# Kernel optimization log

Measured on AMD Instinct MI355X. Metric: run time of the kernel, lower is better.

The kernel has to match this reference:

```python
import jax, jax.numpy as jnp
import numpy as np

B, CIN, COUT, RES, WDIM, K, GN_GROUPS = 8, 512, 512, 64, 512, 3, 32


def setup_inputs() -> dict:
    key = jax.random.key(0)
    ks = jax.random.split(key, 6)
    return dict(
        x=jax.random.normal(ks[0], (B, CIN, RES, RES), jnp.float32),
        w=jax.random.normal(ks[1], (B, WDIM), jnp.float32),
        noise=jax.random.normal(ks[2], (B, 1, RES, RES), jnp.float32),
        weight=jax.random.normal(ks[3], (COUT, CIN, K, K), jnp.float32),
        bias=jnp.zeros((COUT,), jnp.float32),
        affine_W=jax.random.normal(ks[4], (3 * CIN, WDIM), jnp.float32),
        affine_b=jnp.ones((3 * CIN,), jnp.float32),  # bias_init=1
        gn_weight=jnp.ones((CIN,), jnp.float32),
        gn_bias=jnp.zeros((CIN,), jnp.float32),
        gamma=jnp.full((1, COUT, 1, 1), 1e-5, jnp.float32),  # layer_scale_init
        noise_strength=jnp.asarray(0.1, jnp.float32),
    )


def _group_norm_f32(x, weight, bias, groups=GN_GROUPS, eps=1e-5):
    # GroupNorm_float32: normalize in float32, cast back to x.dtype
    b, c, h, w = x.shape
    xf = x.astype(jnp.float32).reshape(b, groups, c // groups, h, w)
    mu = xf.mean(axis=(2, 3, 4), keepdims=True)
    var = xf.var(axis=(2, 3, 4), keepdims=True)
    xn = ((xf - mu) * jax.lax.rsqrt(var + eps)).reshape(b, c, h, w)
    return (xn * weight[None, :, None, None] + bias[None, :, None, None]).astype(x.dtype)


def reference(x, w, noise, weight, bias, affine_W, affine_b, gn_weight, gn_bias, gamma, noise_strength):
    b, cin, h, wd = x.shape
    cout, _, kh, kw = weight.shape
    # StyleSplit: FullyConnectedLayer (weight scaled by 1/sqrt(in_features)) then m1*m2+m3
    s = w @ (affine_W.T / jnp.sqrt(jnp.float32(w.shape[1]))) + affine_b  # [B, 3*Cin]
    m1, m2, m3 = jnp.split(s, 3, axis=1)
    styles = m1 * m2 + m3  # [B, Cin]
    # residual path: GroupNorm (float32) first
    xn = _group_norm_f32(x, gn_weight, gn_bias)
    # modulated_conv2d (fused path): per-sample modulate + demodulate
    wmod = weight[None] * styles[:, None, :, None, None]                 # [B,Cout,Cin,K,K]
    dcoef = jax.lax.rsqrt(jnp.sum(jnp.square(wmod), axis=(2, 3, 4)) + 1e-8)  # [B,Cout]
    wmod = wmod * dcoef[:, :, None, None, None]
    # grouped conv with groups = batch (StyleGAN batch-as-groups trick)
    xg = xn.reshape(1, b * cin, h, wd)
    wg = wmod.reshape(b * cout, cin, kh, kw)
    pad = kh // 2
    y = jax.lax.conv_general_dilated(
        xg, wg, window_strides=(1, 1), padding=[(pad, pad), (pad, pad)],
        dimension_numbers=('NCHW', 'OIHW', 'NCHW'), feature_group_count=b)
    y = y.reshape(b, cout, h, wd)
    # noise injection
    y = y + noise * noise_strength
    # fused bias + lrelu with gain = bias_def_gain['lrelu'] * gain = sqrt(2) * 2
    act_gain = np.sqrt(2.0) * 2.0
    y = jax.nn.leaky_relu(y + bias[None, :, None, None], 0.2) * act_gain
    # layer-scale + residual (residual uses the normalized x) * sqrt(2)
    y = (gamma * y + xn) * np.sqrt(2.0)
    return y
```

## Files before the change

### kernel.cpp

```cpp
#include <hip/hip_runtime.h>
#include <hip/hip_bf16.h>

typedef short short8 __attribute__((ext_vector_type(8)));
typedef float f32x4 __attribute__((ext_vector_type(4)));

#define SWZ(c) (((c) & 3) ^ (((c) >> 2) & 3))

static __device__ __forceinline__ unsigned short f2bf(float f) {
    union { float f; unsigned u; } v; v.f = f;
    unsigned r = v.u + 0x7FFFu + ((v.u >> 16) & 1u);
    return (unsigned short)(r >> 16);
}

static __device__ __forceinline__ void gload16(const void* g, void* l) {
    __builtin_amdgcn_global_load_lds(
        (const __attribute__((address_space(1))) unsigned int*)g,
        (__attribute__((address_space(3))) unsigned int*)l, 16, 0, 0);
}

__global__ __launch_bounds__(256) void stylesk(
    const float* __restrict__ w, const float* __restrict__ affW,
    const float* __restrict__ affb, float* __restrict__ styles)
{
    int ch = blockIdx.x, b = blockIdx.y;
    int lane = threadIdx.x & 63, wv = threadIdx.x >> 6;
    float wr[8];
    const float* wb = w + b * 512 + lane * 8;
#pragma unroll
    for (int r = 0; r < 8; ++r) wr[r] = wb[r];
    for (int ii = 0; ii < 16; ++ii) {
        int i = ch * 64 + wv * 16 + ii;
        float d[3];
#pragma unroll
        for (int jj = 0; jj < 3; ++jj) {
            const float* a = affW + (size_t)(jj * 512 + i) * 512 + lane * 8;
            float dd = 0.f;
#pragma unroll
            for (int r = 0; r < 8; ++r) dd += wr[r] * a[r];
            for (int off = 32; off; off >>= 1) dd += __shfl_xor(dd, off);
            d[jj] = dd;
        }
        if (lane == 0) {
            const float inv = 0.044194173824159216f;
            float s0 = d[0] * inv + affb[i];
            float s1 = d[1] * inv + affb[512 + i];
            float s2 = d[2] * inv + affb[1024 + i];
            styles[b * 512 + i] = s0 * s1 + s2;
        }
    }
}

__global__ __launch_bounds__(256) void gnstats(
    const float* __restrict__ x, float* __restrict__ meanv, float* __restrict__ rstdv)
{
    int bx = blockIdx.x, t = threadIdx.x;
    const float4* p = (const float4*)(x + (size_t)bx * 65536);
    float s = 0.f, q = 0.f;
#pragma unroll 4
    for (int k = 0; k < 64; ++k) {
        float4 v = p[t + (k << 8)];
        s += v.x + v.y + v.z + v.w;
        q += v.x * v.x + v.y * v.y + v.z * v.z + v.w * v.w;
    }
    for (int off = 32; off; off >>= 1) { s += __shfl_xor(s, off); q += __shfl_xor(q, off); }
    __shared__ float rs[4], rq[4];
    if ((t & 63) == 0) { rs[t >> 6] = s; rq[t >> 6] = q; }
    __syncthreads();
    if (t == 0) {
        float S = rs[0] + rs[1] + rs[2] + rs[3];
        float Q = rq[0] + rq[1] + rq[2] + rq[3];
        float mu = S * (1.f / 65536.f);
        float var = Q * (1.f / 65536.f) - mu * mu;
        meanv[bx] = mu;
        rstdv[bx] = rsqrtf(var + 1e-5f);
    }
}

__global__ __launch_bounds__(256) void dcoefk(
    const float* __restrict__ weight, const float* __restrict__ styles,
    float* __restrict__ dcoef)
{
    __shared__ float st2[8 * 512];
    __shared__ float red[32];
    int co = blockIdx.x, t = threadIdx.x;
    for (int i = t; i < 4096; i += 256) { float s = styles[i]; st2[i] = s * s; }
    __syncthreads();
    float p[8] = {0, 0, 0, 0, 0, 0, 0, 0};
#pragma unroll
    for (int half = 0; half < 2; ++half) {
        int ci = t * 2 + half;
        const float* wp = weight + ((size_t)co * 512 + ci) * 9;
        float wsq = 0.f;
#pragma unroll
        for (int k = 0; k < 9; ++k) wsq += wp[k] * wp[k];
#pragma unroll
        for (int b = 0; b < 8; ++b) p[b] += wsq * st2[b * 512 + ci];
    }
    int lane = t & 63, wv = t >> 6;
#pragma unroll
    for (int b = 0; b < 8; ++b) {
        float v = p[b];
        for (int off = 32; off; off >>= 1) v += __shfl_xor(v, off);
        if (lane == 0) red[wv * 8 + b] = v;
    }
    __syncthreads();
    if (t < 8) {
        float s = red[t] + red[8 + t] + red[16 + t] + red[24 + t];
        dcoef[t * 512 + co] = rsqrtf(s + 1e-8f);
    }
}

__global__ __launch_bounds__(256) void packk(
    const float* __restrict__ weight, unsigned short* __restrict__ wpk)
{
    __shared__ float ld[9 * 128];
    int co = blockIdx.x, c4 = blockIdx.y, t = threadIdx.x;
    const float* src = weight + (size_t)co * 4608 + c4 * 1152;
    for (int f = t; f < 1152; f += 256)
        ld[(f % 9) * 128 + (f / 9)] = src[f];
    __syncthreads();
    unsigned short* dst = wpk + (size_t)co * 4608 + c4 * 128;
    for (int f = t; f < 1152; f += 256) {
        int tap = f >> 7, ci = f & 127;
        dst[tap * 512 + ci] = f2bf(ld[tap * 128 + ci]);
    }
}

__global__ __launch_bounds__(256) void modpack(
    const float* __restrict__ x, const float* __restrict__ styles,
    const float* __restrict__ gnw, const float* __restrict__ gnb,
    const float* __restrict__ meanv, const float* __restrict__ rstdv,
    unsigned short* __restrict__ xm)
{
    __shared__ float sA[512], sB[512];
    __shared__ unsigned short tr[32 * 520];
    int t = threadIdx.x;
    int px0 = blockIdx.x * 32, b = blockIdx.y;
    for (int i = t; i < 512; i += 256) {
        int g = i >> 4;
        float mu = meanv[b * 32 + g], r = rstdv[b * 32 + g];
        float st = styles[b * 512 + i];
        float a = r * gnw[i];
        sA[i] = a * st;
        sB[i] = (gnb[i] - mu * a) * st;
    }
    __syncthreads();
    int p = t & 31, cb = t >> 5;
    const float* xb = x + (size_t)b * 512 * 4096 + px0 + p;
#pragma unroll 4
    for (int it = 0; it < 64; ++it) {
        int ci = cb + (it << 3);
        float v = xb[(size_t)ci * 4096];
        tr[p * 520 + ci] = f2bf(v * sA[ci] + sB[ci]);
    }
    __syncthreads();
    int gran = t & 63;
#pragma unroll
    for (int k = 0; k < 8; ++k) {
        int pl = k * 4 + (t >> 6);
        short8 v = *(const short8*)&tr[pl * 520 + gran * 8];
        *(short8*)&xm[((size_t)(b * 4096 + px0 + pl) << 9) + gran * 8] = v;
    }
}

__global__ __launch_bounds__(256, 2) void conv3(
    const unsigned short* __restrict__ xm, const unsigned short* __restrict__ wpk,
    const unsigned short* __restrict__ zp,
    const float* __restrict__ x, const float* __restrict__ noise,
    const float* __restrict__ bias, const float* __restrict__ gnw,
    const float* __restrict__ gnb, const float* __restrict__ gamma,
    const float* __restrict__ dcoef, const float* __restrict__ meanv,
    const float* __restrict__ rstdv, const float* __restrict__ nsp,
    float* __restrict__ out)
{
    __shared__ unsigned short in_lds[4 * 66 * 32];
    __shared__ unsigned short w_lds[3 * 128 * 32];
    const int tid = threadIdx.x, lane = tid & 63, wv = tid >> 6;
    const int ct = blockIdx.x, pt = blockIdx.y, b = blockIdx.z;
    const int co0 = ct * 128;
    const int wm = wv >> 1, wn = wv & 1;
    const int lm = lane & 15, lg = lane >> 4;

    if (tid < 32) {
        int r = tid >> 3, cI = ((tid >> 2) & 1) * 65, g = tid & 3;
        *(short8*)((char*)in_lds + r * 4224 + cI * 64 + g * 16) = (short8)0;
    }

    const int h0 = pt * 2;
    const int imgrow = h0 - 1 + wv;
    const bool rowok = (unsigned)imgrow < 64u;
    const unsigned short* isrc[4];
    char* idst[4];
#pragma unroll
    for (int q = 0; q < 4; ++q) {
        int lin = q * 64 + lane;
        int c1 = lin >> 2, g = lin & 3;
        int gs = g ^ SWZ(c1 + 1);
        isrc[q] = xm + (((size_t)(b * 4096 + imgrow * 64 + c1)) << 9) + gs * 8;
        idst[q] = (char*)in_lds + wv * 4224 + 64 + q * 1024;
    }
    const unsigned short* wsrc[6];
    char* wdst[6];
#pragma unroll
    for (int j = 0; j < 6; ++j) {
        int gid = wv * 384 + j * 64 + lane;
        int dx = gid >> 9, co = (gid >> 2) & 127, g = gid & 3;
        wsrc[j] = wpk + (size_t)(co0 + co) * 4608 + dx * 512 + (g ^ SWZ(co)) * 8;
        wdst[j] = (char*)w_lds + (wv * 384 + j * 64) * 16;
    }

    f32x4 acc[4][4];
#pragma unroll
    for (int m = 0; m < 4; ++m)
#pragma unroll
        for (int n = 0; n < 4; ++n) acc[m][n] = (f32x4){0.f, 0.f, 0.f, 0.f};

    for (int cc = 0; cc < 16; ++cc) {
        __syncthreads();
#pragma unroll
        for (int q = 0; q < 4; ++q)
            gload16(rowok ? (const void*)(isrc[q] + cc * 32) : (const void*)zp, idst[q]);
#pragma unroll
        for (int dy = 0; dy < 3; ++dy) {
            if (dy) __syncthreads();
#pragma unroll
            for (int j = 0; j < 6; ++j)
                gload16(wsrc[j] + dy * 1536 + cc * 32, wdst[j]);
            __syncthreads();
#pragma unroll
            for (int dx = 0; dx < 3; ++dx) {
                short8 af[4], bf[4];
#pragma unroll
                for (int m = 0; m < 4; ++m) {
                    int col = wm * 64 + m * 16 + lm;
                    af[m] = *(const short8*)((char*)w_lds +
                            (dx * 128 + col) * 64 + (lg ^ SWZ(col)) * 16);
                }
#pragma unroll
                for (int n = 0; n < 4; ++n) {
                    int c = n * 16 + lm + dx;
                    bf[n] = *(const short8*)((char*)in_lds +
                            (wn + dy) * 4224 + c * 64 + (lg ^ SWZ(c)) * 16);
                }
#pragma unroll
                for (int m = 0; m < 4; ++m)
#pragma unroll
                    for (int n = 0; n < 4; ++n)
                        acc[m][n] = __builtin_amdgcn_mfma_f32_16x16x32_bf16(
                            af[m], bf[n], acc[m][n], 0, 0, 0);
            }
        }
    }

    const float nsv = *nsp;
#pragma unroll
    for (int m = 0; m < 4; ++m) {
#pragma unroll
        for (int n = 0; n < 4; ++n) {
            int pix = pt * 128 + wn * 64 + n * 16 + lm;
            float nz = noise[b * 4096 + pix] * nsv;
#pragma unroll
            for (int j = 0; j < 4; ++j) {
                int co = co0 + wm * 64 + m * 16 + lg * 4 + j;
                int gidx = co >> 4;
                float v = acc[m][n][j] * dcoef[b * 512 + co] + nz + bias[co];
                float act = (v > 0.f ? v : 0.2f * v) * 2.8284271247461903f;
                float xv = x[((size_t)(b * 512 + co)) * 4096 + pix];
                float xn = (xv - meanv[b * 32 + gidx]) * rstdv[b * 32 + gidx] * gnw[co] + gnb[co];
                out[((size_t)(b * 512 + co)) * 4096 + pix] =
                    (gamma[co] * act + xn) * 1.4142135623730951f;
            }
        }
    }
}

extern "C" void kernel_launch(void* const* d_in, const int* in_sizes, int n_in,
                              void* d_out, int out_size, void* d_ws, size_t ws_size,
                              hipStream_t stream) {
    const float* x      = (const float*)d_in[0];
    const float* w      = (const float*)d_in[1];
    const float* noise  = (const float*)d_in[2];
    const float* weight = (const float*)d_in[3];
    const float* bias   = (const float*)d_in[4];
    const float* affW   = (const float*)d_in[5];
    const float* affb   = (const float*)d_in[6];
    const float* gnw    = (const float*)d_in[7];
    const float* gnb    = (const float*)d_in[8];
    const float* gamma  = (const float*)d_in[9];
    const float* nsp    = (const float*)d_in[10];
    float* out = (float*)d_out;

    char* ws = (char*)d_ws;
    float* styles = (float*)(ws + 0);
    float* dcoef  = (float*)(ws + 16384);
    float* meanv  = (float*)(ws + 32768);
    float* rstdv  = (float*)(ws + 33792);
    unsigned short* zp  = (unsigned short*)(ws + 34816);
    unsigned short* wpk = (unsigned short*)(ws + 38912);
    unsigned short* xm  = (unsigned short*)(ws + 4757504);

    hipMemsetAsync(zp, 0, 4096, stream);

    stylesk<<<dim3(8, 8), 256, 0, stream>>>(w, affW, affb, styles);
    gnstats<<<dim3(256), 256, 0, stream>>>(x, meanv, rstdv);
    packk<<<dim3(512, 4), 256, 0, stream>>>(weight, wpk);
    dcoefk<<<dim3(512), 256, 0, stream>>>(weight, styles, dcoef);
    modpack<<<dim3(128, 8), 256, 0, stream>>>(x, styles, gnw, gnb, meanv, rstdv, xm);
    conv3<<<dim3(4, 32, 8), 256, 0, stream>>>(xm, wpk, zp, x, noise, bias, gnw, gnb,
                                              gamma, dcoef, meanv, rstdv, nsp, out);
}
```

Measured before the change: 337.2 us.

## Enlarge conv tile to eight rows with double-buffered LDS prefetch pipeline

New measurement: 309.5 us. 1.09x faster.

```diff
diff --git a/kernel.cpp b/kernel.cpp
--- a/kernel.cpp
+++ b/kernel.cpp
@@ -22,14 +22,14 @@
     const float* __restrict__ w, const float* __restrict__ affW,
     const float* __restrict__ affb, float* __restrict__ styles)
 {
-    int ch = blockIdx.x, b = blockIdx.y;
+    int bx = blockIdx.x, b = blockIdx.y;
     int lane = threadIdx.x & 63, wv = threadIdx.x >> 6;
     float wr[8];
     const float* wb = w + b * 512 + lane * 8;
 #pragma unroll
     for (int r = 0; r < 8; ++r) wr[r] = wb[r];
-    for (int ii = 0; ii < 16; ++ii) {
-        int i = ch * 64 + wv * 16 + ii;
+    for (int ii = 0; ii < 4; ++ii) {
+        int i = bx * 16 + wv * 4 + ii;
         float d[3];
 #pragma unroll
         for (int jj = 0; jj < 3; ++jj) {
@@ -163,7 +163,7 @@
     }
 }
 
-__global__ __launch_bounds__(256, 2) void conv3(
+__global__ __launch_bounds__(512, 2) void conv3(
     const unsigned short* __restrict__ xm, const unsigned short* __restrict__ wpk,
     const unsigned short* __restrict__ zp,
     const float* __restrict__ x, const float* __restrict__ noise,
@@ -173,91 +173,116 @@
     const float* __restrict__ rstdv, const float* __restrict__ nsp,
     float* __restrict__ out)
 {
-    __shared__ unsigned short in_lds[4 * 66 * 32];
-    __shared__ unsigned short w_lds[3 * 128 * 32];
+    extern __shared__ char smem[];
+    char* wlds = smem;
+    char* ilds = smem + 49152;
+
     const int tid = threadIdx.x, lane = tid & 63, wv = tid >> 6;
     const int ct = blockIdx.x, pt = blockIdx.y, b = blockIdx.z;
-    const int co0 = ct * 128;
-    const int wm = wv >> 1, wn = wv & 1;
+    const int co0 = ct * 128, h0 = pt * 8;
+    const int wm = wv >> 2, wn = wv & 3;
     const int lm = lane & 15, lg = lane >> 4;
 
-    if (tid < 32) {
-        int r = tid >> 3, cI = ((tid >> 2) & 1) * 65, g = tid & 3;
-        *(short8*)((char*)in_lds + r * 4224 + cI * 64 + g * 16) = (short8)0;
-    }
-
-    const int h0 = pt * 2;
-    const int imgrow = h0 - 1 + wv;
-    const bool rowok = (unsigned)imgrow < 64u;
-    const unsigned short* isrc[4];
-    char* idst[4];
-#pragma unroll
-    for (int q = 0; q < 4; ++q) {
-        int lin = q * 64 + lane;
-        int c1 = lin >> 2, g = lin & 3;
-        int gs = g ^ SWZ(c1 + 1);
-        isrc[q] = xm + (((size_t)(b * 4096 + imgrow * 64 + c1)) << 9) + gs * 8;
-        idst[q] = (char*)in_lds + wv * 4224 + 64 + q * 1024;
-    }
-    const unsigned short* wsrc[6];
-    char* wdst[6];
-#pragma unroll
-    for (int j = 0; j < 6; ++j) {
-        int gid = wv * 384 + j * 64 + lane;
-        int dx = gid >> 9, co = (gid >> 2) & 127, g = gid & 3;
-        wsrc[j] = wpk + (size_t)(co0 + co) * 4608 + dx * 512 + (g ^ SWZ(co)) * 8;
-        wdst[j] = (char*)w_lds + (wv * 384 + j * 64) * 16;
-    }
-
-    f32x4 acc[4][4];
+    if (tid < 160) {
+        int sel = tid / 80, rem = tid % 80;
+        int r = rem >> 3, col = ((rem >> 2) & 1) * 65, g = rem & 3;
+        *(short8*)(ilds + sel * 42240 + r * 4224 + col * 64 + g * 16) = (short8)0;
+    }
+
+    const unsigned short* wsrc_fix[3]; int wdst_off[3];
+#pragma unroll
+    for (int q = 0; q < 3; ++q) {
+        int k = q * 8 + wv;
+        int id = k * 64 + lane;
+        int dxid = id >> 9, co = (id >> 2) & 127, g = (id & 3) ^ SWZ(co);
+        wsrc_fix[q] = wpk + (size_t)(co0 + co) * 4608 + dxid * 512 + g * 8;
+        wdst_off[q] = k * 1024;
+    }
+    const unsigned short* isrc_fix[5]; int idst_off[5];
+#pragma unroll
+    for (int q = 0; q < 5; ++q) {
+        int k = q * 8 + wv;
+        int r = k >> 2, chunk = k & 3;
+        int idx = chunk * 64 + lane;
+        int cimg = idx >> 2, gs = (idx & 3) ^ SWZ(cimg + 1);
+        int imgrow = h0 - 1 + r;
+        isrc_fix[q] = ((unsigned)imgrow < 64u)
+            ? xm + (((size_t)(b * 4096 + imgrow * 64 + cimg)) << 9) + gs * 8
+            : zp;
+        idst_off[q] = r * 4224 + 64 + chunk * 1024;
+    }
+
+    int aoff[4];
+#pragma unroll
+    for (int m = 0; m < 4; ++m) {
+        int col = wm * 64 + m * 16 + lm;
+        aoff[m] = col * 64 + (lg ^ SWZ(col)) * 16;
+    }
+    int boff[3][4];
+#pragma unroll
+    for (int dx = 0; dx < 3; ++dx)
+#pragma unroll
+        for (int nc = 0; nc < 4; ++nc) {
+            int c = nc * 16 + lm + dx;
+            boff[dx][nc] = c * 64 + (lg ^ SWZ(c)) * 16;
+        }
+
+    f32x4 acc[4][8];
 #pragma unroll
     for (int m = 0; m < 4; ++m)
 #pragma unroll
-        for (int n = 0; n < 4; ++n) acc[m][n] = (f32x4){0.f, 0.f, 0.f, 0.f};
-
-    for (int cc = 0; cc < 16; ++cc) {
+        for (int n = 0; n < 8; ++n) acc[m][n] = (f32x4){0.f, 0.f, 0.f, 0.f};
+
+#pragma unroll
+    for (int q = 0; q < 3; ++q) gload16(wsrc_fix[q], wlds + wdst_off[q]);
+#pragma unroll
+    for (int q = 0; q < 5; ++q) gload16(isrc_fix[q], ilds + idst_off[q]);
+    __syncthreads();
+
+    int cc = 0, dy = 0;
+    for (int p = 0; p < 48; ++p) {
+        int dyn = dy + 1, ccn = cc;
+        if (dyn == 3) { dyn = 0; ccn = cc + 1; }
+        if (p < 47) {
+            int wadd = dyn * 1536 + ccn * 32;
+            char* wd = wlds + ((p + 1) & 1) * 24576;
+#pragma unroll
+            for (int q = 0; q < 3; ++q) gload16(wsrc_fix[q] + wadd, wd + wdst_off[q]);
+        }
+        if (dy == 0 && cc < 15) {
+            int iadd = (cc + 1) * 32;
+            char* idp = ilds + ((cc + 1) & 1) * 42240;
+#pragma unroll
+            for (int q = 0; q < 5; ++q) gload16(isrc_fix[q] + iadd, idp + idst_off[q]);
+        }
+        char* wbase = wlds + (p & 1) * 24576;
+        char* ibase = ilds + (cc & 1) * 42240 + (2 * wn + dy) * 4224;
+#pragma unroll
+        for (int dx = 0; dx < 3; ++dx) {
+            short8 af[4], bv[8];
+#pragma unroll
+            for (int m = 0; m < 4; ++m)
+                af[m] = *(const short8*)(wbase + dx * 8192 + aoff[m]);
+#pragma unroll
+            for (int n = 0; n < 8; ++n)
+                bv[n] = *(const short8*)(ibase + (n >> 2) * 4224 + boff[dx][n & 3]);
+#pragma unroll
+            for (int m = 0; m < 4; ++m)
+#pragma unroll
+                for (int n = 0; n < 8; ++n)
+                    acc[m][n] = __builtin_amdgcn_mfma_f32_16x16x32_bf16(
+                        af[m], bv[n], acc[m][n], 0, 0, 0);
+        }
         __syncthreads();
-#pragma unroll
-        for (int q = 0; q < 4; ++q)
-            gload16(rowok ? (const void*)(isrc[q] + cc * 32) : (const void*)zp, idst[q]);
-#pragma unroll
-        for (int dy = 0; dy < 3; ++dy) {
-            if (dy) __syncthreads();
-#pragma unroll
-            for (int j = 0; j < 6; ++j)
-                gload16(wsrc[j] + dy * 1536 + cc * 32, wdst[j]);
-            __syncthreads();
-#pragma unroll
-            for (int dx = 0; dx < 3; ++dx) {
-                short8 af[4], bf[4];
-#pragma unroll
-                for (int m = 0; m < 4; ++m) {
-                    int col = wm * 64 + m * 16 + lm;
-                    af[m] = *(const short8*)((char*)w_lds +
-                            (dx * 128 + col) * 64 + (lg ^ SWZ(col)) * 16);
-                }
-#pragma unroll
-                for (int n = 0; n < 4; ++n) {
-                    int c = n * 16 + lm + dx;
-                    bf[n] = *(const short8*)((char*)in_lds +
-                            (wn + dy) * 4224 + c * 64 + (lg ^ SWZ(c)) * 16);
-                }
-#pragma unroll
-                for (int m = 0; m < 4; ++m)
-#pragma unroll
-                    for (int n = 0; n < 4; ++n)
-                        acc[m][n] = __builtin_amdgcn_mfma_f32_16x16x32_bf16(
-                            af[m], bf[n], acc[m][n], 0, 0, 0);
-            }
-        }
+        dy = dyn; cc = ccn;
     }
 
     const float nsv = *nsp;
 #pragma unroll
     for (int m = 0; m < 4; ++m) {
 #pragma unroll
-        for (int n = 0; n < 4; ++n) {
-            int pix = pt * 128 + wn * 64 + n * 16 + lm;
+        for (int n = 0; n < 8; ++n) {
+            int pix = (h0 + 2 * wn + (n >> 2)) * 64 + (n & 3) * 16 + lm;
             float nz = noise[b * 4096 + pix] * nsv;
 #pragma unroll
             for (int j = 0; j < 4; ++j) {
@@ -301,11 +326,14 @@
 
     hipMemsetAsync(zp, 0, 4096, stream);
 
-    stylesk<<<dim3(8, 8), 256, 0, stream>>>(w, affW, affb, styles);
+    hipFuncSetAttribute(reinterpret_cast<const void*>(conv3),
+                        hipFuncAttributeMaxDynamicSharedMemorySize, 135168);
+
+    stylesk<<<dim3(32, 8), 256, 0, stream>>>(w, affW, affb, styles);
     gnstats<<<dim3(256), 256, 0, stream>>>(x, meanv, rstdv);
     packk<<<dim3(512, 4), 256, 0, stream>>>(weight, wpk);
     dcoefk<<<dim3(512), 256, 0, stream>>>(weight, styles, dcoef);
     modpack<<<dim3(128, 8), 256, 0, stream>>>(x, styles, gnw, gnb, meanv, rstdv, xm);
-    conv3<<<dim3(4, 32, 8), 256, 0, stream>>>(xm, wpk, zp, x, noise, bias, gnw, gnb,
-                                              gamma, dcoef, meanv, rstdv, nsp, out);
-}
+    conv3<<<dim3(4, 8, 8), 512, 133632, stream>>>(xm, wpk, zp, x, noise, bias, gnw, gnb,
+                                                  gamma, dcoef, meanv, rstdv, nsp, out);
+}
```
